# Kernel optimization log

Hardware: AMD Instinct MI355X
Metric: run time of the kernel (lower is better)

## Reference

```python
import jax, jax.numpy as jnp
import numpy as np

EMBED_DIM = 1024
NUM_HEADS = 16
D_K = EMBED_DIM // NUM_HEADS
SEQ = 4096
BATCH = 1


def setup_inputs() -> dict:
    key = jax.random.key(0)
    ks = jax.random.split(key, 9)
    s = 1.0 / np.sqrt(EMBED_DIM)
    return {
        "x": jax.random.normal(ks[0], (BATCH, SEQ, EMBED_DIM), dtype=jnp.float32),
        "Wq": jax.random.normal(ks[1], (EMBED_DIM, EMBED_DIM), dtype=jnp.float32) * s,
        "bq": jax.random.normal(ks[2], (EMBED_DIM,), dtype=jnp.float32) * 0.02,
        "Wk": jax.random.normal(ks[3], (EMBED_DIM, EMBED_DIM), dtype=jnp.float32) * s,
        "bk": jax.random.normal(ks[4], (EMBED_DIM,), dtype=jnp.float32) * 0.02,
        "Wv": jax.random.normal(ks[5], (EMBED_DIM, EMBED_DIM), dtype=jnp.float32) * s,
        "bv": jax.random.normal(ks[6], (EMBED_DIM,), dtype=jnp.float32) * 0.02,
        "Wo": jax.random.normal(ks[7], (EMBED_DIM, EMBED_DIM), dtype=jnp.float32) * s,
        "bo": jax.random.normal(ks[8], (EMBED_DIM,), dtype=jnp.float32) * 0.02,
    }


def reference(x, Wq, bq, Wk, bk, Wv, bv, Wo, bo):
    B, S, E = x.shape
    H, Dk = NUM_HEADS, D_K

    def split_heads(t):  # [B,S,E] -> [B,H,S,Dk]
        return t.reshape(B, S, H, Dk).transpose(0, 2, 1, 3)

    Q = split_heads(x @ Wq.T + bq)
    K = split_heads(x @ Wk.T + bk)
    V = split_heads(x @ Wv.T + bv)

    scores = jnp.einsum("bhqd,bhkd->bhqk", Q, K) / jnp.sqrt(jnp.float32(Dk))
    causal = jnp.tril(jnp.ones((S, S), dtype=bool))
    scores = jnp.where(causal, scores, -jnp.inf)
    attn = jax.nn.softmax(scores, axis=-1)
    out = jnp.einsum("bhqk,bhkd->bhqd", attn, V)  # [B,H,S,Dk]
    out = out.transpose(0, 2, 1, 3).reshape(B, S, E)
    return out @ Wo.T + bo
```

## Files before the change

kernel.cpp:

```cpp
#include <hip/hip_runtime.h>
#include <hip/hip_bf16.h>
#include <math.h>

#define SEQ 4096
#define EMB 1024
#define NH  16
#define DK  64

typedef __attribute__((ext_vector_type(8))) unsigned short us8;
typedef __attribute__((ext_vector_type(8))) short         s8;
typedef __attribute__((ext_vector_type(4))) unsigned short us4;
typedef __attribute__((ext_vector_type(4))) float          f4;

static __device__ __forceinline__ unsigned short f2bf(float f) {
    union { float f; unsigned u; } v; v.f = f;
    unsigned r = v.u + 0x7FFF + ((v.u >> 16) & 1);
    return (unsigned short)(r >> 16);
}

__device__ __forceinline__ void gl2lds16(const void* g, void* l) {
    __builtin_amdgcn_global_load_lds((const __attribute__((address_space(1))) void*)g,
                                     (__attribute__((address_space(3))) void*)l, 16, 0, 0);
}

__device__ __forceinline__ int pkbf(float a, float b) {
    return (int)__builtin_amdgcn_perm(__float_as_uint(a), __float_as_uint(b), 0x07060302u);
}

__global__ void cvt_all(const float* __restrict__ x,
                        const float* __restrict__ w0, const float* __restrict__ w1,
                        const float* __restrict__ w2, const float* __restrict__ w3,
                        unsigned short* __restrict__ xo,
                        unsigned short* __restrict__ o0, unsigned short* __restrict__ o1,
                        unsigned short* __restrict__ o2, unsigned short* __restrict__ o3) {
    const int idx = blockIdx.x * 256 + threadIdx.x;
    const float* in;
    unsigned short* out;
    int off;
    if (idx < (1 << 20)) { in = x; out = xo; off = idx; }
    else {
        const int t = idx - (1 << 20);
        const int w = t >> 18;
        off = t & ((1 << 18) - 1);
        in  = w == 0 ? w0 : (w == 1 ? w1 : (w == 2 ? w2 : w3));
        out = w == 0 ? o0 : (w == 1 ? o1 : (w == 2 ? o2 : o3));
    }
    const float4 v = ((const float4*)in)[off];
    us4 o;
    o[0] = f2bf(v.x); o[1] = f2bf(v.y); o[2] = f2bf(v.z); o[3] = f2bf(v.w);
    ((us4*)out)[off] = o;
}

__global__ __launch_bounds__(256) void transpose_kernel(
    const unsigned short* __restrict__ in, unsigned short* __restrict__ out) {
    __shared__ unsigned short t[64][72];
    const int tid = threadIdx.x;
    const int row = tid >> 2, c = (tid & 3) * 16;
    const int gr = blockIdx.x * 64, gc = blockIdx.y * 64;
    const unsigned short* src = in + (size_t)(gr + row) * EMB + gc + c;
    *(us8*)&t[row][c]     = *(const us8*)src;
    *(us8*)&t[row][c + 8] = *(const us8*)(src + 8);
    __syncthreads();
    us8 o0, o1;
#pragma unroll
    for (int j = 0; j < 8; ++j) { o0[j] = t[c + j][row]; o1[j] = t[c + 8 + j][row]; }
    const int a_   = c >> 4;
    const int base = (a_ >> 1) * 32 + (a_ & 1) * 4;
    us4 g0, g1, g2, g3;
#pragma unroll
    for (int i = 0; i < 4; ++i) { g0[i] = o0[i]; g1[i] = o0[4 + i]; g2[i] = o1[i]; g3[i] = o1[4 + i]; }
    unsigned short* dst = out + (size_t)(gc + row) * SEQ + gr + base;
    *(us4*)dst        = g0;
    *(us4*)(dst + 8)  = g1;
    *(us4*)(dst + 16) = g2;
    *(us4*)(dst + 24) = g3;
}

__global__ __launch_bounds__(256) void qkv_gemm(
    const unsigned short* __restrict__ X,
    const unsigned short* __restrict__ Wq, const unsigned short* __restrict__ Wk,
    const unsigned short* __restrict__ Wv,
    const float* __restrict__ bq, const float* __restrict__ bk, const float* __restrict__ bv,
    unsigned short* __restrict__ Qo, unsigned short* __restrict__ Ko, unsigned short* __restrict__ Vo)
{
    __shared__ unsigned short As[128 * 64];
    __shared__ unsigned short Bs[128 * 64];

    const int region = blockIdx.y >> 3;
    const unsigned short* W   = region == 0 ? Wq : (region == 1 ? Wk : Wv);
    const float*         bias = region == 0 ? bq : (region == 1 ? bk : bv);
    unsigned short*      out  = region == 0 ? Qo : (region == 1 ? Ko : Vo);
    const float scale = region == 0 ? 0.18033688011112042f : 1.0f;

    const int tid  = threadIdx.x;
    const int wave = tid >> 6;
    const int lane = tid & 63;
    const int quad = lane >> 4;
    const int l16  = lane & 15;
    const int wm   = (wave >> 1) * 64;
    const int wn   = (wave & 1) * 64;
    const int bm   = blockIdx.x * 128;
    const int bn   = (blockIdx.y & 7) * 128;

    f4 acc[4][4];
#pragma unroll
    for (int a = 0; a < 4; ++a)
#pragma unroll
        for (int b = 0; b < 4; ++b) acc[a][b] = (f4){0, 0, 0, 0};

    const int rsub = lane >> 3;
    const int gc   = ((lane & 7) ^ rsub) * 8;
    const int swz  = l16 & 7;

    for (int k0 = 0; k0 < EMB; k0 += 64) {
        __syncthreads();
#pragma unroll
        for (int i = 0; i < 4; ++i) {
            const int cb = i * 4 + wave;
            const int r  = cb * 8 + rsub;
            gl2lds16(X + (size_t)(bm + r) * EMB + k0 + gc, &As[cb * 512]);
            gl2lds16(W + (size_t)(bn + r) * EMB + k0 + gc, &Bs[cb * 512]);
        }
        __syncthreads();
#pragma unroll
        for (int kc = 0; kc < 2; ++kc) {
            s8 af[4], bf[4];
#pragma unroll
            for (int t = 0; t < 4; ++t) {
                const int seg = (kc * 4 + quad) ^ swz;
                af[t] = *(const s8*)&As[(wm + t * 16 + l16) * 64 + seg * 8];
                bf[t] = *(const s8*)&Bs[(wn + t * 16 + l16) * 64 + seg * 8];
            }
#pragma unroll
            for (int tm = 0; tm < 4; ++tm)
#pragma unroll
                for (int tn = 0; tn < 4; ++tn)
                    acc[tm][tn] = __builtin_amdgcn_mfma_f32_16x16x32_bf16(af[tm], bf[tn], acc[tm][tn], 0, 0, 0);
        }
    }

#pragma unroll
    for (int tn = 0; tn < 4; ++tn) {
        const int n = bn + wn + tn * 16 + l16;
        const float bv2 = bias[n];
#pragma unroll
        for (int tm = 0; tm < 4; ++tm)
#pragma unroll
            for (int rr = 0; rr < 4; ++rr) {
                const int m = bm + wm + tm * 16 + quad * 4 + rr;
                out[(size_t)m * EMB + n] = f2bf((acc[tm][tn][rr] + bv2) * scale);
            }
    }
}

__global__ __launch_bounds__(256) void gemm_op(
    const unsigned short* __restrict__ A, const unsigned short* __restrict__ B,
    const float* __restrict__ bias, float* __restrict__ C)
{
    __shared__ unsigned short As[128 * 64];
    __shared__ unsigned short Bs[64 * 64];

    const int tid  = threadIdx.x;
    const int wave = tid >> 6;
    const int lane = tid & 63;
    const int quad = lane >> 4;
    const int l16  = lane & 15;
    const int wm   = (wave >> 1) * 64;
    const int wn   = (wave & 1) * 32;
    const int bm   = blockIdx.x * 128;
    const int bn   = blockIdx.y * 64;

    f4 acc[4][2];
#pragma unroll
    for (int a = 0; a < 4; ++a) { acc[a][0] = (f4){0,0,0,0}; acc[a][1] = (f4){0,0,0,0}; }

    const int rsub = lane >> 3;
    const int gc   = ((lane & 7) ^ rsub) * 8;
    const int swz  = l16 & 7;

    for (int k0 = 0; k0 < EMB; k0 += 64) {
        __syncthreads();
#pragma unroll
        for (int i = 0; i < 6; ++i) {
            const int cb = i * 4 + wave;
            if (cb < 16) {
                gl2lds16(A + (size_t)(bm + cb * 8 + rsub) * EMB + k0 + gc, &As[cb * 512]);
            } else {
                const int c2 = cb - 16;
                gl2lds16(B + (size_t)(bn + c2 * 8 + rsub) * EMB + k0 + gc, &Bs[c2 * 512]);
            }
        }
        __syncthreads();
#pragma unroll
        for (int kc = 0; kc < 2; ++kc) {
            const int seg = (kc * 4 + quad) ^ swz;
            s8 af[4], bf[2];
#pragma unroll
            for (int t = 0; t < 4; ++t)
                af[t] = *(const s8*)&As[(wm + t * 16 + l16) * 64 + seg * 8];
#pragma unroll
            for (int t = 0; t < 2; ++t)
                bf[t] = *(const s8*)&Bs[(wn + t * 16 + l16) * 64 + seg * 8];
#pragma unroll
            for (int tm = 0; tm < 4; ++tm)
#pragma unroll
                for (int tn = 0; tn < 2; ++tn)
                    acc[tm][tn] = __builtin_amdgcn_mfma_f32_16x16x32_bf16(af[tm], bf[tn], acc[tm][tn], 0, 0, 0);
        }
    }

#pragma unroll
    for (int tn = 0; tn < 2; ++tn) {
        const int n = bn + wn + tn * 16 + l16;
        const float bv2 = bias[n];
#pragma unroll
        for (int tm = 0; tm < 4; ++tm)
#pragma unroll
            for (int rr = 0; rr < 4; ++rr) {
                const int m = bm + wm + tm * 16 + quad * 4 + rr;
                C[(size_t)m * EMB + n] = acc[tm][tn][rr] + bv2;
            }
    }
}

__global__ __launch_bounds__(512, 4) void attn_kernel(
    const unsigned short* __restrict__ Qg, const unsigned short* __restrict__ Kg,
    const unsigned short* __restrict__ Vtg, unsigned short* __restrict__ Og)
{
    __shared__ unsigned short Ks[2][2][64][64];
    __shared__ unsigned short Vs[2][2][64][64];

    const int tid  = threadIdx.x;
    const int wave = tid >> 6;
    const int lane = tid & 63;
    const int quad = lane >> 4;
    const int l16  = lane & 15;
    const int h    = blockIdx.x;
    const int y    = blockIdx.y;
    const int u    = (y < 16) ? y : 47 - y;
    const int jmax = 63 - u;
    const int tileMine = (wave < 4) ? (63 - u) : u;
    const int par  = (wave >> 1) & 1;
    const int qh   = wave & 1;
    const int jmine = tileMine;
    const int colbase = h * DK;
    const int wrow0 = tileMine * 64 + qh * 32;
    const int q0    = wrow0 + l16;

    s8 qf00, qf10, qf01, qf11;
    {
        const unsigned short* q = Qg + (size_t)q0 * EMB + colbase + quad * 8;
        qf00 = *(const s8*)(q);
        qf10 = *(const s8*)(q + 32);
        qf01 = *(const s8*)(q + (size_t)16 * EMB);
        qf11 = *(const s8*)(q + (size_t)16 * EMB + 32);
    }

    const int xr    = (l16 & 7) << 4;
    const int coff0 = ((quad * 16) ^ xr) >> 1;
    const int coff1 = (((64) + quad * 16) ^ xr) >> 1;

    const int srow = tid >> 3;
    const int scol = (((tid & 7) * 16) ^ ((srow & 7) << 4)) >> 1;
    const unsigned short* ksrc = Kg  + (size_t)srow * EMB + colbase + scol;
    const unsigned short* vsrc = Vtg + (size_t)(colbase + srow) * SEQ + scol;

    const int imax = jmax >> 1;

    gl2lds16(ksrc,                    &Ks[0][0][wave * 8][0]);
    gl2lds16(vsrc,                    &Vs[0][0][wave * 8][0]);
    gl2lds16(ksrc + (size_t)64 * EMB, &Ks[0][1][wave * 8][0]);
    gl2lds16(vsrc + 64,               &Vs[0][1][wave * 8][0]);

    float l0 = 0.0f, l1 = 0.0f;
    f4 o0[4], o1[4];
#pragma unroll
    for (int t = 0; t < 4; ++t) { o0[t] = (f4){0, 0, 0, 0}; o1[t] = (f4){0, 0, 0, 0}; }

    for (int i = 0; i <= imax; ++i) {
        __syncthreads();
        const int cur = i & 1;
        if (i < imax) {
            const int nxt = cur ^ 1;
            const int je  = 2 * (i + 1);
            gl2lds16(ksrc + (size_t)je * 64 * EMB, &Ks[nxt][0][wave * 8][0]);
            gl2lds16(vsrc + (size_t)je * 64,       &Vs[nxt][0][wave * 8][0]);
            const int jo = je + 1;
            if (jo <= jmax) {
                gl2lds16(ksrc + (size_t)jo * 64 * EMB, &Ks[nxt][1][wave * 8][0]);
                gl2lds16(vsrc + (size_t)jo * 64,       &Vs[nxt][1][wave * 8][0]);
            }
        }

        const int j = 2 * i + par;
        if (j <= jmine) {
            const unsigned short* KsP = &Ks[cur][par][0][0];
            const unsigned short* VsP = &Vs[cur][par][0][0];

            f4 s0[4] = { {0,0,0,0}, {0,0,0,0}, {0,0,0,0}, {0,0,0,0} };
            f4 s1[4] = { {0,0,0,0}, {0,0,0,0}, {0,0,0,0}, {0,0,0,0} };
            __builtin_amdgcn_s_setprio(1);
#pragma unroll
            for (int t = 0; t < 4; ++t) {
                const int rbase = (t * 16 + l16) * 64;
                s8 kv0 = *(const s8*)&KsP[rbase + coff0];
                s8 kv1 = *(const s8*)&KsP[rbase + coff1];
                s0[t] = __builtin_amdgcn_mfma_f32_16x16x32_bf16(kv0, qf00, s0[t], 0, 0, 0);
                s1[t] = __builtin_amdgcn_mfma_f32_16x16x32_bf16(kv0, qf01, s1[t], 0, 0, 0);
                s0[t] = __builtin_amdgcn_mfma_f32_16x16x32_bf16(kv1, qf10, s0[t], 0, 0, 0);
                s1[t] = __builtin_amdgcn_mfma_f32_16x16x32_bf16(kv1, qf11, s1[t], 0, 0, 0);
            }
            __builtin_amdgcn_s_setprio(0);

            if (j == jmine) {
#pragma unroll
                for (int t = 0; t < 4; ++t) {
                    const int kb = j * 64 + t * 16 + quad * 4;
#pragma unroll
                    for (int r = 0; r < 4; ++r) {
                        if (kb + r > q0)      s0[t][r] = -1e30f;
                        if (kb + r > q0 + 16) s1[t][r] = -1e30f;
                    }
                }
            }

            float rs0 = 0.0f, rs1 = 0.0f;
#pragma unroll
            for (int t = 0; t < 4; ++t)
#pragma unroll
                for (int r = 0; r < 4; ++r) {
                    const float p0 = __builtin_amdgcn_exp2f(s0[t][r]);
                    const float p1 = __builtin_amdgcn_exp2f(s1[t][r]);
                    s0[t][r] = p0; rs0 += p0;
                    s1[t][r] = p1; rs1 += p1;
                }
            rs0 += __shfl_xor(rs0, 16);
            rs0 += __shfl_xor(rs0, 32);
            rs1 += __shfl_xor(rs1, 16);
            rs1 += __shfl_xor(rs1, 32);
            l0 += rs0;
            l1 += rs1;

            union { int i[8]; s8 v[2]; } pk0, pk1;
#pragma unroll
            for (int t = 0; t < 4; ++t) {
                pk0.i[t * 2]     = pkbf(s0[t][1], s0[t][0]);
                pk0.i[t * 2 + 1] = pkbf(s0[t][3], s0[t][2]);
                pk1.i[t * 2]     = pkbf(s1[t][1], s1[t][0]);
                pk1.i[t * 2 + 1] = pkbf(s1[t][3], s1[t][2]);
            }

            __builtin_amdgcn_s_setprio(1);
#pragma unroll
            for (int t = 0; t < 4; ++t) {
                const int rbase = (t * 16 + l16) * 64;
                s8 va0 = *(const s8*)&VsP[rbase + coff0];
                s8 va1 = *(const s8*)&VsP[rbase + coff1];
                o0[t] = __builtin_amdgcn_mfma_f32_16x16x32_bf16(va0, pk0.v[0], o0[t], 0, 0, 0);
                o1[t] = __builtin_amdgcn_mfma_f32_16x16x32_bf16(va0, pk1.v[0], o1[t], 0, 0, 0);
                o0[t] = __builtin_amdgcn_mfma_f32_16x16x32_bf16(va1, pk0.v[1], o0[t], 0, 0, 0);
                o1[t] = __builtin_amdgcn_mfma_f32_16x16x32_bf16(va1, pk1.v[1], o1[t], 0, 0, 0);
            }
            __builtin_amdgcn_s_setprio(0);
        }
    }

    __syncthreads();
    float* mO = (float*)&Ks[0][0][0][0];
    float* mL = (float*)&Vs[0][0][0][0];
    const int slot = (wave >> 2) * 2 + qh;
    const int mrow = slot * 64 + lane;
    char* mp = (char*)mO + (size_t)mrow * 128;
    const int msw = (lane & 7) << 4;
    if (par == 1) {
#pragma unroll
        for (int t = 0; t < 4; ++t) {
            *(f4*)(mp + ((t * 32)      ^ msw)) = o0[t];
            *(f4*)(mp + ((t * 32 + 16) ^ msw)) = o1[t];
        }
        mL[mrow * 2]     = l0;
        mL[mrow * 2 + 1] = l1;
    }
    __syncthreads();
    if (par == 0) {
#pragma unroll
        for (int t = 0; t < 4; ++t) {
            o0[t] += *(const f4*)(mp + ((t * 32)      ^ msw));
            o1[t] += *(const f4*)(mp + ((t * 32 + 16) ^ msw));
        }
        l0 += mL[mrow * 2];
        l1 += mL[mrow * 2 + 1];
        const float inv0 = 1.0f / l0;
        const float inv1 = 1.0f / l1;
#pragma unroll
        for (int t = 0; t < 4; ++t) {
            us4 ov;
#pragma unroll
            for (int r = 0; r < 4; ++r) ov[r] = f2bf(o0[t][r] * inv0);
            *(us4*)&Og[(size_t)q0 * EMB + colbase + t * 16 + quad * 4] = ov;
#pragma unroll
            for (int r = 0; r < 4; ++r) ov[r] = f2bf(o1[t][r] * inv1);
            *(us4*)&Og[(size_t)(q0 + 16) * EMB + colbase + t * 16 + quad * 4] = ov;
        }
    }
}

extern "C" void kernel_launch(void* const* d_in, const int* in_sizes, int n_in,
                              void* d_out, int out_size, void* d_ws, size_t ws_size,
                              hipStream_t stream) {
    const float* x  = (const float*)d_in[0];
    const float* Wq = (const float*)d_in[1];
    const float* bq = (const float*)d_in[2];
    const float* Wk = (const float*)d_in[3];
    const float* bk = (const float*)d_in[4];
    const float* Wv = (const float*)d_in[5];
    const float* bv = (const float*)d_in[6];
    const float* Wo = (const float*)d_in[7];
    const float* bo = (const float*)d_in[8];
    float* out = (float*)d_out;

    unsigned short* ws = (unsigned short*)d_ws;
    unsigned short* xb  = ws;
    unsigned short* Wqb = xb  + (size_t)SEQ * EMB;
    unsigned short* Wkb = Wqb + (size_t)EMB * EMB;
    unsigned short* Wvb = Wkb + (size_t)EMB * EMB;
    unsigned short* Wob = Wvb + (size_t)EMB * EMB;
    unsigned short* Qb  = Wob + (size_t)EMB * EMB;
    unsigned short* Kb  = Qb  + (size_t)SEQ * EMB;
    unsigned short* Vtb = Kb  + (size_t)SEQ * EMB;
    unsigned short* Ab  = Vtb + (size_t)SEQ * EMB;

    cvt_all<<<8192, 256, 0, stream>>>(x, Wq, Wk, Wv, Wo, xb, Wqb, Wkb, Wvb, Wob);

    qkv_gemm<<<dim3(SEQ / 128, 24), 256, 0, stream>>>(xb, Wqb, Wkb, Wvb, bq, bk, bv, Qb, Kb, Ab);

    transpose_kernel<<<dim3(SEQ / 64, EMB / 64), 256, 0, stream>>>(Ab, Vtb);

    attn_kernel<<<dim3(NH, 32), 512, 0, stream>>>(Qb, Kb, Vtb, Ab);

    gemm_op<<<dim3(SEQ / 128, EMB / 64), 256, 0, stream>>>(Ab, Wob, bo, out);
}
```

Before: 199.0 us.

## Rebalance causal attention waves and load V directly from global memory

The attention kernel now reads V fragments straight from global memory into registers instead of staging them in LDS, which frees shared memory and removes half the async copies. After the short tile finishes, the four B-waves are reassigned to help the long tile, splitting its remaining keys three ways. Partial outputs are merged through new LDS buffers. Blocks are also launched on a 1D grid remapped so that each XCD gets contiguous heads. The direct V loads may raise global-memory latency and register pressure, and the extra merge stages add synchronisation.

```diff
diff --git a/kernel.cpp b/kernel.cpp
--- a/kernel.cpp
+++ b/kernel.cpp
@@ -228,24 +228,28 @@
     const unsigned short* __restrict__ Vtg, unsigned short* __restrict__ Og)
 {
     __shared__ unsigned short Ks[2][2][64][64];
-    __shared__ unsigned short Vs[2][2][64][64];
+    __shared__ float mO[8][64][16];
+    __shared__ float mL[8][64];
 
     const int tid  = threadIdx.x;
     const int wave = tid >> 6;
     const int lane = tid & 63;
     const int quad = lane >> 4;
     const int l16  = lane & 15;
-    const int h    = blockIdx.x;
-    const int y    = blockIdx.y;
-    const int u    = (y < 16) ? y : 47 - y;
-    const int jmax = 63 - u;
-    const int tileMine = (wave < 4) ? (63 - u) : u;
-    const int par  = (wave >> 1) & 1;
-    const int qh   = wave & 1;
-    const int jmine = tileMine;
-    const int colbase = h * DK;
-    const int wrow0 = tileMine * 64 + qh * 32;
-    const int q0    = wrow0 + l16;
+
+    const int n      = blockIdx.x;
+    const int workid = (n & 7) * 64 + (n >> 3);
+    const int h      = workid >> 5;
+    const int y      = workid & 31;
+    const int u      = (y < 16) ? y : 47 - y;
+    const int A      = 63 - u;
+    const int par    = (wave >> 1) & 1;
+    const int qh     = wave & 1;
+    const bool isA   = wave < 4;
+    const int tileMine = isA ? A : u;
+    const int jmineLow = isA ? A : u;
+    const int colbase  = h * DK;
+    const int q0       = tileMine * 64 + qh * 32 + l16;
 
     s8 qf00, qf10, qf01, qf11;
     {
@@ -258,47 +262,46 @@
 
     const int xr    = (l16 & 7) << 4;
     const int coff0 = ((quad * 16) ^ xr) >> 1;
-    const int coff1 = (((64) + quad * 16) ^ xr) >> 1;
+    const int coff1 = ((64 + quad * 16) ^ xr) >> 1;
 
     const int srow = tid >> 3;
     const int scol = (((tid & 7) * 16) ^ ((srow & 7) << 4)) >> 1;
-    const unsigned short* ksrc = Kg  + (size_t)srow * EMB + colbase + scol;
-    const unsigned short* vsrc = Vtg + (size_t)(colbase + srow) * SEQ + scol;
-
-    const int imax = jmax >> 1;
+    const unsigned short* ksrc = Kg + (size_t)srow * EMB + colbase + scol;
+
+    const unsigned short* vbase = Vtg + (size_t)(colbase + l16) * SEQ + quad * 8;
+
+    const int iB     = u >> 1;
+    const int ipairs = (65 - u) >> 1;
 
     gl2lds16(ksrc,                    &Ks[0][0][wave * 8][0]);
-    gl2lds16(vsrc,                    &Vs[0][0][wave * 8][0]);
     gl2lds16(ksrc + (size_t)64 * EMB, &Ks[0][1][wave * 8][0]);
-    gl2lds16(vsrc + 64,               &Vs[0][1][wave * 8][0]);
 
     float l0 = 0.0f, l1 = 0.0f;
     f4 o0[4], o1[4];
 #pragma unroll
     for (int t = 0; t < 4; ++t) { o0[t] = (f4){0, 0, 0, 0}; o1[t] = (f4){0, 0, 0, 0}; }
 
-    for (int i = 0; i <= imax; ++i) {
+    for (int i = 0; i <= iB; ++i) {
         __syncthreads();
         const int cur = i & 1;
-        if (i < imax) {
-            const int nxt = cur ^ 1;
-            const int je  = 2 * (i + 1);
-            gl2lds16(ksrc + (size_t)je * 64 * EMB, &Ks[nxt][0][wave * 8][0]);
-            gl2lds16(vsrc + (size_t)je * 64,       &Vs[nxt][0][wave * 8][0]);
-            const int jo = je + 1;
-            if (jo <= jmax) {
-                gl2lds16(ksrc + (size_t)jo * 64 * EMB, &Ks[nxt][1][wave * 8][0]);
-                gl2lds16(vsrc + (size_t)jo * 64,       &Vs[nxt][1][wave * 8][0]);
-            }
-        }
-
+        if (i + 1 < ipairs) {
+            const int je = 2 * (i + 1);
+            gl2lds16(ksrc + (size_t)je * 64 * EMB, &Ks[cur ^ 1][0][wave * 8][0]);
+            if (je + 1 <= A)
+                gl2lds16(ksrc + (size_t)(je + 1) * 64 * EMB, &Ks[cur ^ 1][1][wave * 8][0]);
+        }
         const int j = 2 * i + par;
-        if (j <= jmine) {
-            const unsigned short* KsP = &Ks[cur][par][0][0];
-            const unsigned short* VsP = &Vs[cur][par][0][0];
-
+        if (j <= jmineLow) {
+            s8 va0[4], va1[4];
+            const unsigned short* vj = vbase + j * 64;
+#pragma unroll
+            for (int t = 0; t < 4; ++t) {
+                va0[t] = *(const s8*)(vj + (size_t)(t * 16) * SEQ);
+                va1[t] = *(const s8*)(vj + (size_t)(t * 16) * SEQ + 32);
+            }
             f4 s0[4] = { {0,0,0,0}, {0,0,0,0}, {0,0,0,0}, {0,0,0,0} };
             f4 s1[4] = { {0,0,0,0}, {0,0,0,0}, {0,0,0,0}, {0,0,0,0} };
+            const unsigned short* KsP = &Ks[cur][par][0][0];
             __builtin_amdgcn_s_setprio(1);
 #pragma unroll
             for (int t = 0; t < 4; ++t) {
@@ -312,7 +315,7 @@
             }
             __builtin_amdgcn_s_setprio(0);
 
-            if (j == jmine) {
+            if (j == jmineLow) {
 #pragma unroll
                 for (int t = 0; t < 4; ++t) {
                     const int kb = j * 64 + t * 16 + quad * 4;
@@ -353,54 +356,162 @@
             __builtin_amdgcn_s_setprio(1);
 #pragma unroll
             for (int t = 0; t < 4; ++t) {
+                o0[t] = __builtin_amdgcn_mfma_f32_16x16x32_bf16(va0[t], pk0.v[0], o0[t], 0, 0, 0);
+                o1[t] = __builtin_amdgcn_mfma_f32_16x16x32_bf16(va0[t], pk1.v[0], o1[t], 0, 0, 0);
+                o0[t] = __builtin_amdgcn_mfma_f32_16x16x32_bf16(va1[t], pk0.v[1], o0[t], 0, 0, 0);
+                o1[t] = __builtin_amdgcn_mfma_f32_16x16x32_bf16(va1[t], pk1.v[1], o1[t], 0, 0, 0);
+            }
+            __builtin_amdgcn_s_setprio(0);
+        }
+    }
+
+    if (wave >= 6) {
+        const int hs = (wave - 6) * 2;
+        f4* hp0 = (f4*)&mO[hs][lane][0];
+        hp0[0] = o0[0]; hp0[1] = o0[1]; hp0[2] = o0[2]; hp0[3] = o0[3];
+        mL[hs][lane] = l0;
+        f4* hp1 = (f4*)&mO[hs + 1][lane][0];
+        hp1[0] = o1[0]; hp1[1] = o1[1]; hp1[2] = o1[2]; hp1[3] = o1[3];
+        mL[hs + 1][lane] = l1;
+    }
+    __syncthreads();
+    if (wave == 4 || wave == 5) {
+        const int hs = (wave - 4) * 2;
+        const f4* hp0 = (const f4*)&mO[hs][lane][0];
+        const f4* hp1 = (const f4*)&mO[hs + 1][lane][0];
+        const float inv0 = 1.0f / (l0 + mL[hs][lane]);
+        const float inv1 = 1.0f / (l1 + mL[hs + 1][lane]);
+#pragma unroll
+        for (int t = 0; t < 4; ++t) {
+            f4 a = o0[t] + hp0[t];
+            f4 b = o1[t] + hp1[t];
+            us4 ov;
+#pragma unroll
+            for (int r = 0; r < 4; ++r) ov[r] = f2bf(a[r] * inv0);
+            *(us4*)&Og[(size_t)q0 * EMB + colbase + t * 16 + quad * 4] = ov;
+#pragma unroll
+            for (int r = 0; r < 4; ++r) ov[r] = f2bf(b[r] * inv1);
+            *(us4*)&Og[(size_t)(q0 + 16) * EMB + colbase + t * 16 + quad * 4] = ov;
+        }
+    }
+    int qrowH, parH;
+    if (isA) {
+        parH = 0;
+        qrowH = A * 64 + qh * 32 + par * 16 + l16;
+        if (par) {
+#pragma unroll
+            for (int t = 0; t < 4; ++t) { f4 tmp = o0[t]; o0[t] = o1[t]; o1[t] = tmp; }
+            const float tl = l0; l0 = l1; l1 = tl;
+            qf00 = qf01; qf10 = qf11;
+        }
+    } else {
+        parH = 1;
+        const int b  = wave - 4;
+        const int cB = ((b & 1) << 1) | (b >> 1);
+        qrowH = A * 64 + cB * 16 + l16;
+        const unsigned short* q = Qg + (size_t)qrowH * EMB + colbase + quad * 8;
+        qf00 = *(const s8*)(q);
+        qf10 = *(const s8*)(q + 32);
+#pragma unroll
+        for (int t = 0; t < 4; ++t) o0[t] = (f4){0, 0, 0, 0};
+        l0 = 0.0f;
+    }
+
+    for (int i = iB + 1; i < ipairs; ++i) {
+        __syncthreads();
+        const int cur = i & 1;
+        if (i + 1 < ipairs) {
+            const int je = 2 * (i + 1);
+            gl2lds16(ksrc + (size_t)je * 64 * EMB, &Ks[cur ^ 1][0][wave * 8][0]);
+            if (je + 1 <= A)
+                gl2lds16(ksrc + (size_t)(je + 1) * 64 * EMB, &Ks[cur ^ 1][1][wave * 8][0]);
+        }
+        const int j = 2 * i + parH;
+        if (j <= A) {
+            s8 va0[4], va1[4];
+            const unsigned short* vj = vbase + j * 64;
+#pragma unroll
+            for (int t = 0; t < 4; ++t) {
+                va0[t] = *(const s8*)(vj + (size_t)(t * 16) * SEQ);
+                va1[t] = *(const s8*)(vj + (size_t)(t * 16) * SEQ + 32);
+            }
+            f4 sh[4] = { {0,0,0,0}, {0,0,0,0}, {0,0,0,0}, {0,0,0,0} };
+            const unsigned short* KsP = &Ks[cur][parH][0][0];
+            __builtin_amdgcn_s_setprio(1);
+#pragma unroll
+            for (int t = 0; t < 4; ++t) {
                 const int rbase = (t * 16 + l16) * 64;
-                s8 va0 = *(const s8*)&VsP[rbase + coff0];
-                s8 va1 = *(const s8*)&VsP[rbase + coff1];
-                o0[t] = __builtin_amdgcn_mfma_f32_16x16x32_bf16(va0, pk0.v[0], o0[t], 0, 0, 0);
-                o1[t] = __builtin_amdgcn_mfma_f32_16x16x32_bf16(va0, pk1.v[0], o1[t], 0, 0, 0);
-                o0[t] = __builtin_amdgcn_mfma_f32_16x16x32_bf16(va1, pk0.v[1], o0[t], 0, 0, 0);
-                o1[t] = __builtin_amdgcn_mfma_f32_16x16x32_bf16(va1, pk1.v[1], o1[t], 0, 0, 0);
+                s8 kv0 = *(const s8*)&KsP[rbase + coff0];
+                s8 kv1 = *(const s8*)&KsP[rbase + coff1];
+                sh[t] = __builtin_amdgcn_mfma_f32_16x16x32_bf16(kv0, qf00, sh[t], 0, 0, 0);
+                sh[t] = __builtin_amdgcn_mfma_f32_16x16x32_bf16(kv1, qf10, sh[t], 0, 0, 0);
             }
             __builtin_amdgcn_s_setprio(0);
-        }
-    }
-
+
+            if (j == A) {
+#pragma unroll
+                for (int t = 0; t < 4; ++t) {
+                    const int kb = j * 64 + t * 16 + quad * 4;
+#pragma unroll
+                    for (int r = 0; r < 4; ++r)
+                        if (kb + r > qrowH) sh[t][r] = -1e30f;
+                }
+            }
+
+            float rs = 0.0f;
+#pragma unroll
+            for (int t = 0; t < 4; ++t)
+#pragma unroll
+                for (int r = 0; r < 4; ++r) {
+                    const float p = __builtin_amdgcn_exp2f(sh[t][r]);
+                    sh[t][r] = p;
+                    rs += p;
+                }
+            rs += __shfl_xor(rs, 16);
+            rs += __shfl_xor(rs, 32);
+            l0 += rs;
+
+            union { int i[8]; s8 v[2]; } pkH;
+#pragma unroll
+            for (int t = 0; t < 4; ++t) {
+                pkH.i[t * 2]     = pkbf(sh[t][1], sh[t][0]);
+                pkH.i[t * 2 + 1] = pkbf(sh[t][3], sh[t][2]);
+            }
+
+            __builtin_amdgcn_s_setprio(1);
+#pragma unroll
+            for (int t = 0; t < 4; ++t) {
+                o0[t] = __builtin_amdgcn_mfma_f32_16x16x32_bf16(va0[t], pkH.v[0], o0[t], 0, 0, 0);
+                o0[t] = __builtin_amdgcn_mfma_f32_16x16x32_bf16(va1[t], pkH.v[1], o0[t], 0, 0, 0);
+            }
+            __builtin_amdgcn_s_setprio(0);
+        }
+    }
+
+    if (isA) {
+        f4* hp = (f4*)&mO[wave][lane][0];
+        hp[0] = o1[0]; hp[1] = o1[1]; hp[2] = o1[2]; hp[3] = o1[3];
+        mL[wave][lane] = l1;
+    } else {
+        const int b  = wave - 4;
+        const int cB = ((b & 1) << 1) | (b >> 1);
+        f4* hp = (f4*)&mO[4 + cB][lane][0];
+        hp[0] = o0[0]; hp[1] = o0[1]; hp[2] = o0[2]; hp[3] = o0[3];
+        mL[4 + cB][lane] = l0;
+    }
     __syncthreads();
-    float* mO = (float*)&Ks[0][0][0][0];
-    float* mL = (float*)&Vs[0][0][0][0];
-    const int slot = (wave >> 2) * 2 + qh;
-    const int mrow = slot * 64 + lane;
-    char* mp = (char*)mO + (size_t)mrow * 128;
-    const int msw = (lane & 7) << 4;
-    if (par == 1) {
+    if (isA) {
+        const int cOwn = qh * 2 + par;
+        const f4* fp = (const f4*)&mO[wave ^ 2][lane][0];
+        const f4* bp = (const f4*)&mO[4 + cOwn][lane][0];
+        const float inv = 1.0f / (l0 + mL[wave ^ 2][lane] + mL[4 + cOwn][lane]);
 #pragma unroll
         for (int t = 0; t < 4; ++t) {
-            *(f4*)(mp + ((t * 32)      ^ msw)) = o0[t];
-            *(f4*)(mp + ((t * 32 + 16) ^ msw)) = o1[t];
-        }
-        mL[mrow * 2]     = l0;
-        mL[mrow * 2 + 1] = l1;
-    }
-    __syncthreads();
-    if (par == 0) {
-#pragma unroll
-        for (int t = 0; t < 4; ++t) {
-            o0[t] += *(const f4*)(mp + ((t * 32)      ^ msw));
-            o1[t] += *(const f4*)(mp + ((t * 32 + 16) ^ msw));
-        }
-        l0 += mL[mrow * 2];
-        l1 += mL[mrow * 2 + 1];
-        const float inv0 = 1.0f / l0;
-        const float inv1 = 1.0f / l1;
-#pragma unroll
-        for (int t = 0; t < 4; ++t) {
+            f4 v = o0[t] + fp[t] + bp[t];
             us4 ov;
 #pragma unroll
-            for (int r = 0; r < 4; ++r) ov[r] = f2bf(o0[t][r] * inv0);
-            *(us4*)&Og[(size_t)q0 * EMB + colbase + t * 16 + quad * 4] = ov;
-#pragma unroll
-            for (int r = 0; r < 4; ++r) ov[r] = f2bf(o1[t][r] * inv1);
-            *(us4*)&Og[(size_t)(q0 + 16) * EMB + colbase + t * 16 + quad * 4] = ov;
+            for (int r = 0; r < 4; ++r) ov[r] = f2bf(v[r] * inv);
+            *(us4*)&Og[(size_t)qrowH * EMB + colbase + t * 16 + quad * 4] = ov;
         }
     }
 }
@@ -436,7 +547,7 @@
 
     transpose_kernel<<<dim3(SEQ / 64, EMB / 64), 256, 0, stream>>>(Ab, Vtb);
 
-    attn_kernel<<<dim3(NH, 32), 512, 0, stream>>>(Qb, Kb, Vtb, Ab);
+    attn_kernel<<<512, 512, 0, stream>>>(Qb, Kb, Vtb, Ab);
 
     gemm_op<<<dim3(SEQ / 128, EMB / 64), 256, 0, stream>>>(Ab, Wob, bo, out);
 }
```

New measurement: 321.4 us. 1.62x slower.

## Remap attention blocks to adjacent tile pairs with XCD-aware head placement

Applied to the files above, without the earlier changes.

Switches the attention launch to a 1D grid. Block indices are decoded so each XCD handles two heads, which keeps that head's K/V in the XCD-local L2. Each block now processes adjacent query tiles (2g, 2g+1) instead of pairing u with 63-u. Heavy blocks are issued in the first round and light ones later, for longest-first scheduling. Because the paired tiles share K/V prefix loads, the odd-tile check goes away. The merge through LDS now uses a per-element strided layout instead of swizzled f4 stores. This may cause bank-conflict or instruction overhead and gives less even per-block balance than the old pairing.

```diff
diff --git a/kernel.cpp b/kernel.cpp
--- a/kernel.cpp
+++ b/kernel.cpp
@@ -235,17 +235,25 @@
     const int lane = tid & 63;
     const int quad = lane >> 4;
     const int l16  = lane & 15;
-    const int h    = blockIdx.x;
-    const int y    = blockIdx.y;
-    const int u    = (y < 16) ? y : 47 - y;
-    const int jmax = 63 - u;
-    const int tileMine = (wave < 4) ? (63 - u) : u;
+
+    const int b   = blockIdx.x;
+    const int xcd = b & 7;
+    const int i6  = b >> 3;
+    const int rnd = i6 >> 5;
+    const int i5  = i6 & 31;
+    const int h   = xcd * 2 + (i5 >> 4);
+    const int i4  = i5 & 15;
+    const int g   = rnd ? i4 : 31 - i4;
+    const int tA  = 2 * g + 1;
+    const int tB  = 2 * g;
+
     const int par  = (wave >> 1) & 1;
     const int qh   = wave & 1;
-    const int jmine = tileMine;
-    const int colbase = h * DK;
-    const int wrow0 = tileMine * 64 + qh * 32;
-    const int q0    = wrow0 + l16;
+    const bool isA = wave < 4;
+    const int tileMine = isA ? tA : tB;
+    const int jmine    = tileMine;
+    const int colbase  = h * DK;
+    const int q0       = tileMine * 64 + qh * 32 + l16;
 
     s8 qf00, qf10, qf01, qf11;
     {
@@ -258,15 +266,13 @@
 
     const int xr    = (l16 & 7) << 4;
     const int coff0 = ((quad * 16) ^ xr) >> 1;
-    const int coff1 = (((64) + quad * 16) ^ xr) >> 1;
+    const int coff1 = ((64 + quad * 16) ^ xr) >> 1;
 
     const int srow = tid >> 3;
     const int scol = (((tid & 7) * 16) ^ ((srow & 7) << 4)) >> 1;
     const unsigned short* ksrc = Kg  + (size_t)srow * EMB + colbase + scol;
     const unsigned short* vsrc = Vtg + (size_t)(colbase + srow) * SEQ + scol;
 
-    const int imax = jmax >> 1;
-
     gl2lds16(ksrc,                    &Ks[0][0][wave * 8][0]);
     gl2lds16(vsrc,                    &Vs[0][0][wave * 8][0]);
     gl2lds16(ksrc + (size_t)64 * EMB, &Ks[0][1][wave * 8][0]);
@@ -277,21 +283,16 @@
 #pragma unroll
     for (int t = 0; t < 4; ++t) { o0[t] = (f4){0, 0, 0, 0}; o1[t] = (f4){0, 0, 0, 0}; }
 
-    for (int i = 0; i <= imax; ++i) {
+    for (int i = 0; i <= g; ++i) {
         __syncthreads();
         const int cur = i & 1;
-        if (i < imax) {
-            const int nxt = cur ^ 1;
-            const int je  = 2 * (i + 1);
-            gl2lds16(ksrc + (size_t)je * 64 * EMB, &Ks[nxt][0][wave * 8][0]);
-            gl2lds16(vsrc + (size_t)je * 64,       &Vs[nxt][0][wave * 8][0]);
-            const int jo = je + 1;
-            if (jo <= jmax) {
-                gl2lds16(ksrc + (size_t)jo * 64 * EMB, &Ks[nxt][1][wave * 8][0]);
-                gl2lds16(vsrc + (size_t)jo * 64,       &Vs[nxt][1][wave * 8][0]);
-            }
-        }
-
+        if (i < g) {
+            const int je = 2 * (i + 1);
+            gl2lds16(ksrc + (size_t)je * 64 * EMB,       &Ks[cur ^ 1][0][wave * 8][0]);
+            gl2lds16(vsrc + (size_t)je * 64,             &Vs[cur ^ 1][0][wave * 8][0]);
+            gl2lds16(ksrc + (size_t)(je + 1) * 64 * EMB, &Ks[cur ^ 1][1][wave * 8][0]);
+            gl2lds16(vsrc + (size_t)(je + 1) * 64,       &Vs[cur ^ 1][1][wave * 8][0]);
+        }
         const int j = 2 * i + par;
         if (j <= jmine) {
             const unsigned short* KsP = &Ks[cur][par][0][0];
@@ -366,40 +367,34 @@
     }
 
     __syncthreads();
-    float* mO = (float*)&Ks[0][0][0][0];
-    float* mL = (float*)&Vs[0][0][0][0];
-    const int slot = (wave >> 2) * 2 + qh;
-    const int mrow = slot * 64 + lane;
-    char* mp = (char*)mO + (size_t)mrow * 128;
-    const int msw = (lane & 7) << 4;
+    float* mO8 = (float*)&Ks[0][0][0][0];
+    float* mL8 = (float*)&Vs[0][0][0][0];
+    const int slot0 = (isA ? 0 : 4) + qh * 2;
     if (par == 1) {
 #pragma unroll
-        for (int t = 0; t < 4; ++t) {
-            *(f4*)(mp + ((t * 32)      ^ msw)) = o0[t];
-            *(f4*)(mp + ((t * 32 + 16) ^ msw)) = o1[t];
-        }
-        mL[mrow * 2]     = l0;
-        mL[mrow * 2 + 1] = l1;
+        for (int t = 0; t < 4; ++t)
+#pragma unroll
+            for (int r = 0; r < 4; ++r) {
+                mO8[(slot0       * 16 + t * 4 + r) * 64 + lane] = o0[t][r];
+                mO8[((slot0 + 1) * 16 + t * 4 + r) * 64 + lane] = o1[t][r];
+            }
+        mL8[slot0 * 64 + lane]       = l0;
+        mL8[(slot0 + 1) * 64 + lane] = l1;
     }
     __syncthreads();
     if (par == 0) {
-#pragma unroll
-        for (int t = 0; t < 4; ++t) {
-            o0[t] += *(const f4*)(mp + ((t * 32)      ^ msw));
-            o1[t] += *(const f4*)(mp + ((t * 32 + 16) ^ msw));
-        }
-        l0 += mL[mrow * 2];
-        l1 += mL[mrow * 2 + 1];
-        const float inv0 = 1.0f / l0;
-        const float inv1 = 1.0f / l1;
+        const float inv0 = 1.0f / (l0 + mL8[slot0 * 64 + lane]);
+        const float inv1 = 1.0f / (l1 + mL8[(slot0 + 1) * 64 + lane]);
 #pragma unroll
         for (int t = 0; t < 4; ++t) {
             us4 ov;
 #pragma unroll
-            for (int r = 0; r < 4; ++r) ov[r] = f2bf(o0[t][r] * inv0);
+            for (int r = 0; r < 4; ++r)
+                ov[r] = f2bf((o0[t][r] + mO8[(slot0 * 16 + t * 4 + r) * 64 + lane]) * inv0);
             *(us4*)&Og[(size_t)q0 * EMB + colbase + t * 16 + quad * 4] = ov;
 #pragma unroll
-            for (int r = 0; r < 4; ++r) ov[r] = f2bf(o1[t][r] * inv1);
+            for (int r = 0; r < 4; ++r)
+                ov[r] = f2bf((o1[t][r] + mO8[((slot0 + 1) * 16 + t * 4 + r) * 64 + lane]) * inv1);
             *(us4*)&Og[(size_t)(q0 + 16) * EMB + colbase + t * 16 + quad * 4] = ov;
         }
     }
@@ -436,7 +431,7 @@
 
     transpose_kernel<<<dim3(SEQ / 64, EMB / 64), 256, 0, stream>>>(Ab, Vtb);
 
-    attn_kernel<<<dim3(NH, 32), 512, 0, stream>>>(Qb, Kb, Vtb, Ab);
+    attn_kernel<<<512, 512, 0, stream>>>(Qb, Kb, Vtb, Ab);
 
     gemm_op<<<dim3(SEQ / 128, EMB / 64), 256, 0, stream>>>(Ab, Wob, bo, out);
 }
```

Result: slower. 210.7 us (+5.8%).

## Fuse V transpose into QKV GEMM epilogue and remap blocks for XCD locality

Applied to the files above, without the earlier changes.

The V projection now writes its output directly in the transposed, interleaved layout the attention kernel expects, so the separate transpose kernel launch and its extra read and write of V are removed. Both GEMM kernels also remap their flat block index so that consecutive blocks in the dispatch order (which round-robins across 8 chiplets) land on neighbouring tiles, improving L2 reuse per chiplet. The transposed V stores are 8-byte scattered writes with a large stride, which may coalesce poorly.

```diff
diff --git a/kernel.cpp b/kernel.cpp
--- a/kernel.cpp
+++ b/kernel.cpp
@@ -51,45 +51,24 @@
     ((us4*)out)[off] = o;
 }
 
-__global__ __launch_bounds__(256) void transpose_kernel(
-    const unsigned short* __restrict__ in, unsigned short* __restrict__ out) {
-    __shared__ unsigned short t[64][72];
-    const int tid = threadIdx.x;
-    const int row = tid >> 2, c = (tid & 3) * 16;
-    const int gr = blockIdx.x * 64, gc = blockIdx.y * 64;
-    const unsigned short* src = in + (size_t)(gr + row) * EMB + gc + c;
-    *(us8*)&t[row][c]     = *(const us8*)src;
-    *(us8*)&t[row][c + 8] = *(const us8*)(src + 8);
-    __syncthreads();
-    us8 o0, o1;
-#pragma unroll
-    for (int j = 0; j < 8; ++j) { o0[j] = t[c + j][row]; o1[j] = t[c + 8 + j][row]; }
-    const int a_   = c >> 4;
-    const int base = (a_ >> 1) * 32 + (a_ & 1) * 4;
-    us4 g0, g1, g2, g3;
-#pragma unroll
-    for (int i = 0; i < 4; ++i) { g0[i] = o0[i]; g1[i] = o0[4 + i]; g2[i] = o1[i]; g3[i] = o1[4 + i]; }
-    unsigned short* dst = out + (size_t)(gc + row) * SEQ + gr + base;
-    *(us4*)dst        = g0;
-    *(us4*)(dst + 8)  = g1;
-    *(us4*)(dst + 16) = g2;
-    *(us4*)(dst + 24) = g3;
-}
-
 __global__ __launch_bounds__(256) void qkv_gemm(
     const unsigned short* __restrict__ X,
     const unsigned short* __restrict__ Wq, const unsigned short* __restrict__ Wk,
     const unsigned short* __restrict__ Wv,
     const float* __restrict__ bq, const float* __restrict__ bk, const float* __restrict__ bv,
-    unsigned short* __restrict__ Qo, unsigned short* __restrict__ Ko, unsigned short* __restrict__ Vo)
+    unsigned short* __restrict__ Qo, unsigned short* __restrict__ Ko, unsigned short* __restrict__ Vto)
 {
     __shared__ unsigned short As[128 * 64];
     __shared__ unsigned short Bs[128 * 64];
 
-    const int region = blockIdx.y >> 3;
+    const int flat = blockIdx.y * 32 + blockIdx.x;
+    const int wg   = (flat & 7) * 96 + (flat >> 3);
+    const int bxi  = wg & 31;
+    const int byi  = wg >> 5;
+
+    const int region = byi >> 3;
     const unsigned short* W   = region == 0 ? Wq : (region == 1 ? Wk : Wv);
     const float*         bias = region == 0 ? bq : (region == 1 ? bk : bv);
-    unsigned short*      out  = region == 0 ? Qo : (region == 1 ? Ko : Vo);
     const float scale = region == 0 ? 0.18033688011112042f : 1.0f;
 
     const int tid  = threadIdx.x;
@@ -99,8 +78,8 @@
     const int l16  = lane & 15;
     const int wm   = (wave >> 1) * 64;
     const int wn   = (wave & 1) * 64;
-    const int bm   = blockIdx.x * 128;
-    const int bn   = (blockIdx.y & 7) * 128;
+    const int bm   = bxi * 128;
+    const int bn   = (byi & 7) * 128;
 
     f4 acc[4][4];
 #pragma unroll
@@ -139,17 +118,34 @@
         }
     }
 
-#pragma unroll
-    for (int tn = 0; tn < 4; ++tn) {
-        const int n = bn + wn + tn * 16 + l16;
-        const float bv2 = bias[n];
-#pragma unroll
-        for (int tm = 0; tm < 4; ++tm)
-#pragma unroll
-            for (int rr = 0; rr < 4; ++rr) {
-                const int m = bm + wm + tm * 16 + quad * 4 + rr;
-                out[(size_t)m * EMB + n] = f2bf((acc[tm][tn][rr] + bv2) * scale);
-            }
+    if (region == 2) {
+#pragma unroll
+        for (int tn = 0; tn < 4; ++tn) {
+            const int n = bn + wn + tn * 16 + l16;
+            const float bv2 = bias[n];
+#pragma unroll
+            for (int tm = 0; tm < 4; ++tm) {
+                us4 ov;
+#pragma unroll
+                for (int rr = 0; rr < 4; ++rr) ov[rr] = f2bf(acc[tm][tn][rr] + bv2);
+                const int pos = (tm >> 1) * 32 + quad * 8 + (tm & 1) * 4;
+                *(us4*)&Vto[(size_t)n * SEQ + bm + (wm & 64) + pos] = ov;
+            }
+        }
+    } else {
+#pragma unroll
+        for (int tn = 0; tn < 4; ++tn) {
+            const int n = bn + wn + tn * 16 + l16;
+            const float bv2 = bias[n];
+            unsigned short* out = region == 0 ? Qo : Ko;
+#pragma unroll
+            for (int tm = 0; tm < 4; ++tm)
+#pragma unroll
+                for (int rr = 0; rr < 4; ++rr) {
+                    const int m = bm + wm + tm * 16 + quad * 4 + rr;
+                    out[(size_t)m * EMB + n] = f2bf((acc[tm][tn][rr] + bv2) * scale);
+                }
+        }
     }
 }
 
@@ -159,6 +155,11 @@
 {
     __shared__ unsigned short As[128 * 64];
     __shared__ unsigned short Bs[64 * 64];
+
+    const int flat = blockIdx.y * 32 + blockIdx.x;
+    const int wg   = (flat & 7) * 64 + (flat >> 3);
+    const int bxi  = wg & 31;
+    const int byi  = wg >> 5;
 
     const int tid  = threadIdx.x;
     const int wave = tid >> 6;
@@ -167,8 +168,8 @@
     const int l16  = lane & 15;
     const int wm   = (wave >> 1) * 64;
     const int wn   = (wave & 1) * 32;
-    const int bm   = blockIdx.x * 128;
-    const int bn   = blockIdx.y * 64;
+    const int bm   = bxi * 128;
+    const int bn   = byi * 64;
 
     f4 acc[4][2];
 #pragma unroll
@@ -432,9 +433,7 @@
 
     cvt_all<<<8192, 256, 0, stream>>>(x, Wq, Wk, Wv, Wo, xb, Wqb, Wkb, Wvb, Wob);
 
-    qkv_gemm<<<dim3(SEQ / 128, 24), 256, 0, stream>>>(xb, Wqb, Wkb, Wvb, bq, bk, bv, Qb, Kb, Ab);
-
-    transpose_kernel<<<dim3(SEQ / 64, EMB / 64), 256, 0, stream>>>(Ab, Vtb);
+    qkv_gemm<<<dim3(SEQ / 128, 24), 256, 0, stream>>>(xb, Wqb, Wkb, Wvb, bq, bk, bv, Qb, Kb, Vtb);
 
     attn_kernel<<<dim3(NH, 32), 512, 0, stream>>>(Qb, Kb, Vtb, Ab);
 
```

After: 198.6 us. Within noise of the previous version (-0.2%).
